# Kernel tuning notes

Measured on AMD Instinct MI355X. Metric: run time of the kernel, lower is better.

Reference implementation:

```python
import jax, jax.numpy as jnp
import numpy as np

COST_CLASS = 1.0
COST_MASK = 5.0
COST_DICE = 5.0


def _sample_points(masks, coords):
    """Bilinear grid_sample (align_corners=False, zero padding).

    masks:  [N, H, W] float
    coords: [P, 2] in [0, 1], (x, y) order as in torch grid_sample
    returns [N, P]
    """
    H, W = masks.shape[-2], masks.shape[-1]
    # torch: grid = 2*c - 1; pixel = ((grid+1)*size - 1)/2 = c*size - 0.5
    x = coords[:, 0] * W - 0.5
    y = coords[:, 1] * H - 0.5
    x0 = jnp.floor(x)
    y0 = jnp.floor(y)
    tx = (x - x0).astype(masks.dtype)
    ty = (y - y0).astype(masks.dtype)
    x0i = x0.astype(jnp.int32)
    y0i = y0.astype(jnp.int32)

    def gather(ix, iy):
        valid = ((ix >= 0) & (ix < W) & (iy >= 0) & (iy < H)).astype(masks.dtype)
        v = masks[:, jnp.clip(iy, 0, H - 1), jnp.clip(ix, 0, W - 1)]  # [N, P]
        return v * valid

    v00 = gather(x0i, y0i)
    v01 = gather(x0i + 1, y0i)
    v10 = gather(x0i, y0i + 1)
    v11 = gather(x0i + 1, y0i + 1)
    return (v00 * (1 - tx) * (1 - ty) + v01 * tx * (1 - ty)
            + v10 * (1 - tx) * ty + v11 * tx * ty)


def _cost_one(pred_mask, pred_logits, tgt_mask, labels, coords):
    # pred_mask [Q,H,W], pred_logits [Q,C], tgt_mask [T,H,W], labels [T], coords [P,2]
    probs = jax.nn.softmax(pred_logits, axis=-1)          # [Q, C]
    cost_class = -probs[:, labels]                        # [Q, T]

    pm = _sample_points(pred_mask, coords)                # [Q, P] logits
    tm = _sample_points(tgt_mask, coords)                 # [T, P] in [0,1]
    P = pm.shape[1]

    # pair-wise sigmoid BCE: BCE(x, 1) = softplus(-x), BCE(x, 0) = softplus(x)
    ce_pos = jax.nn.softplus(-pm) / P                     # [Q, P]
    ce_neg = jax.nn.softplus(pm) / P                      # [Q, P]
    cost_mask = ce_pos @ tm.T + ce_neg @ (1.0 - tm).T     # [Q, T]

    # pair-wise dice
    sig = jax.nn.sigmoid(pm)                              # [Q, P]
    numerator = 2.0 * (sig @ tm.T)                        # [Q, T]
    denominator = sig.sum(-1)[:, None] + tm.sum(-1)[None, :]
    cost_dice = 1.0 - (numerator + 1.0) / (denominator + 1.0)

    return COST_MASK * cost_mask + COST_CLASS * cost_class + COST_DICE * cost_dice


def setup_inputs() -> dict:
    key = jax.random.key(0)
    k1, k2, k3, k4, k5 = jax.random.split(key, 5)
    B, Q, C, T, H, W, P = 8, 150, 134, 32, 160, 160, 12544
    masks_queries_logits = jax.random.normal(k1, (B, Q, H, W), dtype=jnp.float32)
    class_queries_logits = jax.random.normal(k2, (B, Q, C), dtype=jnp.float32)
    # binary target masks
    mask_labels = (jax.random.uniform(k3, (B, T, H, W)) > 0.5).astype(jnp.float32)
    class_labels = jax.random.randint(k4, (B, T), 0, 133, dtype=jnp.int64)
    point_coords = jax.random.uniform(k5, (B, P, 2), dtype=jnp.float32)
    return {
        "masks_queries_logits": masks_queries_logits,
        "class_queries_logits": class_queries_logits,
        "mask_labels": mask_labels,
        "class_labels": class_labels,
        "point_coords": point_coords,
    }


def reference(masks_queries_logits, class_queries_logits, mask_labels, class_labels, point_coords):
    # Returns the per-sample cost matrices [B, Q, T] (the GPU-side work of the
    # matcher). The scipy Hungarian assignment on these matrices is CPU-bound
    # and intentionally excluded from the kernel baseline.
    cost = jax.vmap(_cost_one)(
        masks_queries_logits, class_queries_logits, mask_labels, class_labels, point_coords
    )
    return cost
```

## Files before the change

### kernel.cpp

```cpp
#include <hip/hip_runtime.h>
#include <hip/hip_bf16.h>
#include <hip/hip_fp16.h>
#include <math.h>

#define B_ 8
#define Q_ 150
#define QP_ 160
#define C_ 134
#define T_ 32
#define H_ 160
#define W_ 160
#define P_ 12544
#define HW_ (H_ * W_)
#define HW4_ (HW_ / 4)

#define SBLK 1024
#define SBATCH 3
#define STAIL 256
#define SEG_ 56
#define KSEG 224
#define KITER 7
#define DSTRIDE (2 * B_ * QP_ * T_)

typedef __attribute__((ext_vector_type(8))) short short8;
typedef __attribute__((ext_vector_type(4))) float floatx4;

struct Samp {
  int i00, i01, i10, i11;
  float w00, w01, w10, w11;
};

__device__ __forceinline__ Samp make_samp(float cx, float cy) {
  float x = cx * (float)W_ - 0.5f;
  float y = cy * (float)H_ - 0.5f;
  float x0f = floorf(x), y0f = floorf(y);
  float tx = x - x0f, ty = y - y0f;
  int x0 = (int)x0f, y0 = (int)y0f;
  int x1 = x0 + 1, y1 = y0 + 1;
  bool vx0 = (x0 >= 0) && (x0 < W_);
  bool vx1 = (x1 >= 0) && (x1 < W_);
  bool vy0 = (y0 >= 0) && (y0 < H_);
  bool vy1 = (y1 >= 0) && (y1 < H_);
  int cx0 = min(max(x0, 0), W_ - 1), cx1 = min(max(x1, 0), W_ - 1);
  int cy0 = min(max(y0, 0), H_ - 1), cy1 = min(max(y1, 0), H_ - 1);
  Samp s;
  s.i00 = cy0 * W_ + cx0;
  s.i01 = cy0 * W_ + cx1;
  s.i10 = cy1 * W_ + cx0;
  s.i11 = cy1 * W_ + cx1;
  float w00 = (1.f - tx) * (1.f - ty);
  float w01 = tx * (1.f - ty);
  float w10 = (1.f - tx) * ty;
  float w11 = tx * ty;
  s.w00 = (vx0 && vy0) ? w00 : 0.f;
  s.w01 = (vx1 && vy0) ? w01 : 0.f;
  s.w10 = (vx0 && vy1) ? w10 : 0.f;
  s.w11 = (vx1 && vy1) ? w11 : 0.f;
  return s;
}

__device__ __forceinline__ float waveSum(float v) {
#pragma unroll
  for (int m = 32; m >= 1; m >>= 1) v += __shfl_xor(v, m, 64);
  return v;
}
__device__ __forceinline__ float waveMax(float v) {
#pragma unroll
  for (int m = 32; m >= 1; m >>= 1) v = fmaxf(v, __shfl_xor(v, m, 64));
  return v;
}

__device__ __forceinline__ unsigned short f2bf(float x) {
  union { __hip_bfloat16 h; unsigned short u; } cv;
  cv.h = __float2bfloat16(x);
  return cv.u;
}
__device__ __forceinline__ float bf2f(unsigned short u) {
  return __uint_as_float(((unsigned int)u) << 16);
}
__device__ __forceinline__ float h2f(unsigned short u) {
  union { __half h; unsigned short u; } cv;
  cv.u = u;
  return __half2float(cv.h);
}
__device__ __forceinline__ unsigned short f2h(float x) {
  union { __half h; unsigned short u; } cv;
  cv.h = __float2half(x);
  return cv.u;
}

__launch_bounds__(256) __global__
void samp_kernel(const float* __restrict__ coords,
                 unsigned int* __restrict__ sIdx,
                 uint2* __restrict__ sW) {
  int i = blockIdx.x * 256 + threadIdx.x;
  float2 cc = ((const float2*)coords)[i];
  Samp s = make_samp(cc.x, cc.y);
  int dx = s.i01 - s.i00;
  int dy = (s.i10 != s.i00) ? 1 : 0;
  sIdx[i] = (unsigned)s.i00 | ((unsigned)dx << 15) | ((unsigned)dy << 16);
  uint2 w;
  w.x = (unsigned)f2h(s.w00) | ((unsigned)f2h(s.w01) << 16);
  w.y = (unsigned)f2h(s.w10) | ((unsigned)f2h(s.w11) << 16);
  sW[i] = w;
}

__device__ __forceinline__ float lds_sample(const unsigned short* img,
                                            unsigned iv, uint2 wv) {
  int i00 = iv & 0x7fff;
  int i01 = i00 + ((iv >> 15) & 1);
  int ir = (iv & 0x10000) ? W_ : 0;
  return h2f(wv.x & 0xffff) * bf2f(img[i00]) +
         h2f(wv.x >> 16) * bf2f(img[i01]) +
         h2f(wv.y & 0xffff) * bf2f(img[i00 + ir]) +
         h2f(wv.y >> 16) * bf2f(img[i01 + ir]);
}

__launch_bounds__(SBLK, 8) __global__
void sample_kernel(const float* __restrict__ masks_q,
                   const float* __restrict__ mask_labels,
                   const unsigned int* __restrict__ sIdx,
                   const uint2* __restrict__ sW,
                   unsigned short* __restrict__ pmh,
                   unsigned short* __restrict__ tmh,
                   float* __restrict__ S_sp, float* __restrict__ S_sig,
                   float* __restrict__ S_tm) {
  __shared__ unsigned short img[HW_];
  __shared__ float red[32];
  const int x = blockIdx.x;
  const int b = blockIdx.y;
  const int tid = threadIdx.x;
  const bool isPm = (x < Q_);

  const float* src = isPm ? (masks_q + ((size_t)b * Q_ + x) * HW_)
                          : (mask_labels + ((size_t)b * T_ + (x - Q_)) * HW_);
  const float4* s4 = (const float4*)src;
#pragma unroll
  for (int c = 0; c < 6; ++c) {
    int i = c * SBLK + tid;
    float4 v = s4[i];
    ushort4 u;
    u.x = f2bf(v.x); u.y = f2bf(v.y); u.z = f2bf(v.z); u.w = f2bf(v.w);
    *(ushort4*)&img[4 * i] = u;
  }
  if (tid < HW4_ - 6 * SBLK) {
    int i = 6 * SBLK + tid;
    float4 v = s4[i];
    ushort4 u;
    u.x = f2bf(v.x); u.y = f2bf(v.y); u.z = f2bf(v.z); u.w = f2bf(v.w);
    *(ushort4*)&img[4 * i] = u;
  }
  __syncthreads();

  const unsigned int* sIdxB = sIdx + (size_t)b * P_;
  const uint2* sWB = sW + (size_t)b * P_;

  if (isPm) {
    unsigned short* dst = pmh + ((size_t)b * QP_ + x) * P_;
    float ssp = 0.f, ssg = 0.f;
    for (int c = 0; c < SBATCH; ++c) {
      int p = c * (4 * SBLK) + tid;
      unsigned iv[4];
      uint2 wv[4];
      float v[4];
#pragma unroll
      for (int j = 0; j < 4; ++j) {
        iv[j] = sIdxB[p + j * SBLK];
        wv[j] = sWB[p + j * SBLK];
      }
#pragma unroll
      for (int j = 0; j < 4; ++j) v[j] = lds_sample(img, iv[j], wv[j]);
#pragma unroll
      for (int j = 0; j < 4; ++j) {
        float pm = v[j];
        float e = __expf(-fabsf(pm));
        float r = __builtin_amdgcn_rcpf(1.f + e);
        float sp = fmaxf(pm, 0.f) - __logf(r);
        float sg = (pm >= 0.f) ? r : e * r;
        ssp += sp;
        ssg += sg;
        dst[p + j * SBLK] = f2bf(pm);
      }
    }
    if (tid < STAIL) {
      int p = SBATCH * 4 * SBLK + tid;
      float pm = lds_sample(img, sIdxB[p], sWB[p]);
      float e = __expf(-fabsf(pm));
      float r = __builtin_amdgcn_rcpf(1.f + e);
      float sp = fmaxf(pm, 0.f) - __logf(r);
      float sg = (pm >= 0.f) ? r : e * r;
      ssp += sp;
      ssg += sg;
      dst[p] = f2bf(pm);
    }
    ssp = waveSum(ssp);
    ssg = waveSum(ssg);
    int w = tid >> 6;
    if ((tid & 63) == 0) {
      red[w] = ssp;
      red[16 + w] = ssg;
    }
    __syncthreads();
    if (tid == 0) {
      float a = 0.f, bb = 0.f;
#pragma unroll
      for (int i = 0; i < 16; ++i) { a += red[i]; bb += red[16 + i]; }
      S_sp[b * Q_ + x] = a;
      S_sig[b * Q_ + x] = bb;
    }
  } else {
    const int t = x - Q_;
    unsigned short* dst = tmh + ((size_t)b * T_ + t) * P_;
    float stm = 0.f;
    for (int c = 0; c < SBATCH; ++c) {
      int p = c * (4 * SBLK) + tid;
      unsigned iv[4];
      uint2 wv[4];
#pragma unroll
      for (int j = 0; j < 4; ++j) {
        iv[j] = sIdxB[p + j * SBLK];
        wv[j] = sWB[p + j * SBLK];
      }
#pragma unroll
      for (int j = 0; j < 4; ++j) {
        float v = lds_sample(img, iv[j], wv[j]);
        stm += v;
        dst[p + j * SBLK] = f2bf(v);
      }
    }
    if (tid < STAIL) {
      int p = SBATCH * 4 * SBLK + tid;
      float v = lds_sample(img, sIdxB[p], sWB[p]);
      stm += v;
      dst[p] = f2bf(v);
    }
    stm = waveSum(stm);
    int w = tid >> 6;
    if ((tid & 63) == 0) red[w] = stm;
    __syncthreads();
    if (tid == 0) {
      float a = 0.f;
#pragma unroll
      for (int i = 0; i < 16; ++i) a += red[i];
      S_tm[b * T_ + t] = a;
    }
  }
}

__device__ __forceinline__ short8 sig_frag(short8 a) {
  short8 out;
#pragma unroll
  for (int j = 0; j < 8; ++j) {
    float x = bf2f((unsigned short)a[j]);
    float e = __expf(-fabsf(x));
    float r = __builtin_amdgcn_rcpf(1.f + e);
    float sg = (x >= 0.f) ? r : e * r;
    out[j] = (short)f2bf(sg);
  }
  return out;
}

__launch_bounds__(320) __global__
void gemm_kernel(const unsigned short* __restrict__ pmh,
                 const unsigned short* __restrict__ tmh,
                 float* __restrict__ accP) {
  const int b = blockIdx.y;
  const int seg = blockIdx.x;
  const int w = threadIdx.x >> 6;
  const int l = threadIdx.x & 63;
  const int quad = l >> 4;
  const int mrow = l & 15;

  const unsigned short* pmb = pmh + ((size_t)b * QP_ + w * 32) * P_;
  const unsigned short* tmb = tmh + (size_t)b * T_ * P_;

  floatx4 aL[2][2];
  floatx4 aS[2][2];
#pragma unroll
  for (int i = 0; i < 2; ++i)
#pragma unroll
    for (int j = 0; j < 2; ++j) {
      aL[i][j] = (floatx4){0.f, 0.f, 0.f, 0.f};
      aS[i][j] = (floatx4){0.f, 0.f, 0.f, 0.f};
    }

  const int kbase = seg * KSEG;
#pragma unroll
  for (int ki = 0; ki < KITER; ++ki) {
    const int k0 = kbase + ki * 32 + quad * 8;
    short8 a0 = *(const short8*)(pmb + (size_t)(0 * 16 + mrow) * P_ + k0);
    short8 a1 = *(const short8*)(pmb + (size_t)(1 * 16 + mrow) * P_ + k0);
    short8 b0 = *(const short8*)(tmb + (size_t)(0 * 16 + mrow) * P_ + k0);
    short8 b1 = *(const short8*)(tmb + (size_t)(1 * 16 + mrow) * P_ + k0);
    short8 s0 = sig_frag(a0);
    short8 s1 = sig_frag(a1);
    aL[0][0] = __builtin_amdgcn_mfma_f32_16x16x32_bf16(a0, b0, aL[0][0], 0, 0, 0);
    aL[0][1] = __builtin_amdgcn_mfma_f32_16x16x32_bf16(a0, b1, aL[0][1], 0, 0, 0);
    aL[1][0] = __builtin_amdgcn_mfma_f32_16x16x32_bf16(a1, b0, aL[1][0], 0, 0, 0);
    aL[1][1] = __builtin_amdgcn_mfma_f32_16x16x32_bf16(a1, b1, aL[1][1], 0, 0, 0);
    aS[0][0] = __builtin_amdgcn_mfma_f32_16x16x32_bf16(s0, b0, aS[0][0], 0, 0, 0);
    aS[0][1] = __builtin_amdgcn_mfma_f32_16x16x32_bf16(s0, b1, aS[0][1], 0, 0, 0);
    aS[1][0] = __builtin_amdgcn_mfma_f32_16x16x32_bf16(s1, b0, aS[1][0], 0, 0, 0);
    aS[1][1] = __builtin_amdgcn_mfma_f32_16x16x32_bf16(s1, b1, aS[1][1], 0, 0, 0);
  }

  float* base = accP + (size_t)seg * DSTRIDE;
#pragma unroll
  for (int mtl = 0; mtl < 2; ++mtl)
#pragma unroll
    for (int nt = 0; nt < 2; ++nt)
#pragma unroll
      for (int r = 0; r < 4; ++r) {
        int q = w * 32 + mtl * 16 + quad * 4 + r;
        int t = nt * 16 + mrow;
        base[((size_t)(0 * B_ + b) * QP_ + q) * T_ + t] = aL[mtl][nt][r];
        base[((size_t)(1 * B_ + b) * QP_ + q) * T_ + t] = aS[mtl][nt][r];
      }
}

__launch_bounds__(256) __global__
void reduce_kernel(const float* __restrict__ accP, float* __restrict__ accD) {
  int i = blockIdx.x * 256 + threadIdx.x;
  float s = 0.f;
#pragma unroll
  for (int seg = 0; seg < SEG_; ++seg) s += accP[(size_t)seg * DSTRIDE + i];
  accD[i] = s;
}

__launch_bounds__(64) __global__
void final_kernel(const float* __restrict__ class_q,
                  const int* __restrict__ labels,
                  const float* __restrict__ accD,
                  const float* __restrict__ S_sp,
                  const float* __restrict__ S_sig,
                  const float* __restrict__ S_tm,
                  float* __restrict__ out) {
  const int bq = blockIdx.x;
  const int b = bq / Q_;
  const int q = bq % Q_;
  const int l = threadIdx.x;
  const float* cl = class_q + (size_t)bq * C_;

  float v = -INFINITY;
  for (int c = l; c < C_; c += 64) v = fmaxf(v, cl[c]);
  float m = waveMax(v);
  float e = 0.f;
  for (int c = l; c < C_; c += 64) e += __expf(cl[c] - m);
  float den = waveSum(e);

  if (l < T_) {
    int t = l;
    int lbl = labels[b * T_ + t];
    float prob = __expf(cl[lbl] - m) / den;
    float Dlin = accD[((size_t)(0 * B_ + b) * QP_ + q) * T_ + t];
    float Dsig = accD[((size_t)(1 * B_ + b) * QP_ + q) * T_ + t];
    float cmask = (S_sp[bq] - Dlin) * (1.f / (float)P_);
    float dice = 1.f - (2.f * Dsig + 1.f) / (S_sig[bq] + S_tm[b * T_ + t] + 1.f);
    out[(size_t)bq * T_ + t] = 5.f * cmask + 5.f * dice - prob;
  }
}

extern "C" void kernel_launch(void* const* d_in, const int* in_sizes, int n_in,
                              void* d_out, int out_size, void* d_ws,
                              size_t ws_size, hipStream_t stream) {
  const float* masks_q = (const float*)d_in[0];
  const float* class_q = (const float*)d_in[1];
  const float* mask_labels = (const float*)d_in[2];
  const int* class_labels = (const int*)d_in[3];
  const float* coords = (const float*)d_in[4];
  float* out = (float*)d_out;

  float* accD = (float*)d_ws;
  float* accP = accD + DSTRIDE;
  uint2* sW = (uint2*)(accP + (size_t)SEG_ * DSTRIDE);
  unsigned int* sIdx = (unsigned int*)(sW + (size_t)B_ * P_);
  float* S_sp = (float*)(sIdx + (size_t)B_ * P_);
  float* S_sig = S_sp + B_ * Q_;
  float* S_tm = S_sig + B_ * Q_;
  unsigned short* pmh = (unsigned short*)(S_tm + B_ * T_);
  unsigned short* tmh = pmh + (size_t)B_ * QP_ * P_;

  samp_kernel<<<(B_ * P_) / 256, 256, 0, stream>>>(coords, sIdx, sW);
  sample_kernel<<<dim3(Q_ + T_, B_), SBLK, 0, stream>>>(
      masks_q, mask_labels, sIdx, sW, pmh, tmh, S_sp, S_sig, S_tm);
  gemm_kernel<<<dim3(SEG_, B_), 320, 0, stream>>>(pmh, tmh, accP);
  reduce_kernel<<<DSTRIDE / 256, 256, 0, stream>>>(accP, accD);
  final_kernel<<<B_ * Q_, 64, 0, stream>>>(class_q, class_labels, accD, S_sp,
                                           S_sig, S_tm, out);
}
```

Baseline: 238.2 us.

## Store shifted bf16 image copy in LDS so bilinear taps need two 32-bit reads

The sample kernel now writes two bf16 copies of each mask into LDS, one shifted by a single element. Each horizontal pair of bilinear taps can then be fetched with one aligned 32-bit load, so a sample needs two LDS reads instead of four 16-bit reads. Sampling metadata is packed into a single uint4 holding a precomputed byte offset and the half-precision weights. The kernel also loads all 12 packed entries up front. The cost is double the LDS per block (about 100KB), which lowers occupancy (launch bound 8 down to 4), plus extra global reads while staging the image.

```diff
diff --git a/kernel.cpp b/kernel.cpp
--- a/kernel.cpp
+++ b/kernel.cpp
@@ -15,8 +15,9 @@
 #define HW4_ (HW_ / 4)
 
 #define SBLK 1024
-#define SBATCH 3
+#define NPT 12
 #define STAIL 256
+#define BOFS 51200
 #define SEG_ 56
 #define KSEG 224
 #define KITER 7
@@ -25,40 +26,6 @@
 typedef __attribute__((ext_vector_type(8))) short short8;
 typedef __attribute__((ext_vector_type(4))) float floatx4;
 
-struct Samp {
-  int i00, i01, i10, i11;
-  float w00, w01, w10, w11;
-};
-
-__device__ __forceinline__ Samp make_samp(float cx, float cy) {
-  float x = cx * (float)W_ - 0.5f;
-  float y = cy * (float)H_ - 0.5f;
-  float x0f = floorf(x), y0f = floorf(y);
-  float tx = x - x0f, ty = y - y0f;
-  int x0 = (int)x0f, y0 = (int)y0f;
-  int x1 = x0 + 1, y1 = y0 + 1;
-  bool vx0 = (x0 >= 0) && (x0 < W_);
-  bool vx1 = (x1 >= 0) && (x1 < W_);
-  bool vy0 = (y0 >= 0) && (y0 < H_);
-  bool vy1 = (y1 >= 0) && (y1 < H_);
-  int cx0 = min(max(x0, 0), W_ - 1), cx1 = min(max(x1, 0), W_ - 1);
-  int cy0 = min(max(y0, 0), H_ - 1), cy1 = min(max(y1, 0), H_ - 1);
-  Samp s;
-  s.i00 = cy0 * W_ + cx0;
-  s.i01 = cy0 * W_ + cx1;
-  s.i10 = cy1 * W_ + cx0;
-  s.i11 = cy1 * W_ + cx1;
-  float w00 = (1.f - tx) * (1.f - ty);
-  float w01 = tx * (1.f - ty);
-  float w10 = (1.f - tx) * ty;
-  float w11 = tx * ty;
-  s.w00 = (vx0 && vy0) ? w00 : 0.f;
-  s.w01 = (vx1 && vy0) ? w01 : 0.f;
-  s.w10 = (vx0 && vy1) ? w10 : 0.f;
-  s.w11 = (vx1 && vy1) ? w11 : 0.f;
-  return s;
-}
-
 __device__ __forceinline__ float waveSum(float v) {
 #pragma unroll
   for (int m = 32; m >= 1; m >>= 1) v += __shfl_xor(v, m, 64);
@@ -78,9 +45,9 @@
 __device__ __forceinline__ float bf2f(unsigned short u) {
   return __uint_as_float(((unsigned int)u) << 16);
 }
-__device__ __forceinline__ float h2f(unsigned short u) {
+__device__ __forceinline__ float h2f(unsigned u) {
   union { __half h; unsigned short u; } cv;
-  cv.u = u;
+  cv.u = (unsigned short)u;
   return __half2float(cv.h);
 }
 __device__ __forceinline__ unsigned short f2h(float x) {
@@ -91,41 +58,63 @@
 
 __launch_bounds__(256) __global__
 void samp_kernel(const float* __restrict__ coords,
-                 unsigned int* __restrict__ sIdx,
-                 uint2* __restrict__ sW) {
+                 uint4* __restrict__ sPack) {
   int i = blockIdx.x * 256 + threadIdx.x;
   float2 cc = ((const float2*)coords)[i];
-  Samp s = make_samp(cc.x, cc.y);
-  int dx = s.i01 - s.i00;
-  int dy = (s.i10 != s.i00) ? 1 : 0;
-  sIdx[i] = (unsigned)s.i00 | ((unsigned)dx << 15) | ((unsigned)dy << 16);
-  uint2 w;
-  w.x = (unsigned)f2h(s.w00) | ((unsigned)f2h(s.w01) << 16);
-  w.y = (unsigned)f2h(s.w10) | ((unsigned)f2h(s.w11) << 16);
-  sW[i] = w;
-}
-
-__device__ __forceinline__ float lds_sample(const unsigned short* img,
-                                            unsigned iv, uint2 wv) {
-  int i00 = iv & 0x7fff;
-  int i01 = i00 + ((iv >> 15) & 1);
-  int ir = (iv & 0x10000) ? W_ : 0;
-  return h2f(wv.x & 0xffff) * bf2f(img[i00]) +
-         h2f(wv.x >> 16) * bf2f(img[i01]) +
-         h2f(wv.y & 0xffff) * bf2f(img[i00 + ir]) +
-         h2f(wv.y >> 16) * bf2f(img[i01 + ir]);
-}
-
-__launch_bounds__(SBLK, 8) __global__
+  float x = cc.x * (float)W_ - 0.5f;
+  float y = cc.y * (float)H_ - 0.5f;
+  float x0f = floorf(x), y0f = floorf(y);
+  float tx = x - x0f, ty = y - y0f;
+  int x0 = (int)x0f, y0 = (int)y0f;
+
+  bool vx0 = (x0 >= 0) && (x0 < W_);
+  bool vx1 = (x0 + 1 >= 0) && (x0 + 1 < W_);
+  int bx; float wx0, wx1;
+  if (vx0) { bx = x0; wx0 = 1.f - tx; wx1 = vx1 ? tx : 0.f; }
+  else     { bx = min(max(x0 + 1, 0), W_ - 1); wx0 = vx1 ? tx : 0.f; wx1 = 0.f; }
+
+  bool vy0 = (y0 >= 0) && (y0 < H_);
+  bool vy1 = (y0 + 1 >= 0) && (y0 + 1 < H_);
+  int by, ir; float wy0, wy1;
+  if (vy0) {
+    by = y0; wy0 = 1.f - ty;
+    if (vy1) { wy1 = ty; ir = 1; } else { wy1 = 0.f; ir = 0; }
+  } else {
+    by = min(max(y0 + 1, 0), H_ - 1); wy0 = vy1 ? ty : 0.f; wy1 = 0.f; ir = 0;
+  }
+
+  int pi = by * W_ + bx;
+  unsigned off0 = (unsigned)((pi >> 1) * 4 + (pi & 1) * BOFS);
+  uint4 u;
+  u.x = off0 | (ir ? (320u << 17) : 0u);
+  u.y = (unsigned)f2h(wx0 * wy0) | ((unsigned)f2h(wx1 * wy0) << 16);
+  u.z = (unsigned)f2h(wx0 * wy1) | ((unsigned)f2h(wx1 * wy1) << 16);
+  u.w = 0u;
+  sPack[i] = u;
+}
+
+__device__ __forceinline__ float lds2(const unsigned short* img, uint4 pk) {
+  unsigned off0 = pk.x & 0x1ffffu;
+  unsigned off1 = off0 + (pk.x >> 17);
+  unsigned p0 = *(const unsigned*)((const char*)img + off0);
+  unsigned p1 = *(const unsigned*)((const char*)img + off1);
+  float v00 = __uint_as_float(p0 << 16);
+  float v01 = __uint_as_float(p0 & 0xffff0000u);
+  float v10 = __uint_as_float(p1 << 16);
+  float v11 = __uint_as_float(p1 & 0xffff0000u);
+  return h2f(pk.y & 0xffffu) * v00 + h2f(pk.y >> 16) * v01 +
+         h2f(pk.z & 0xffffu) * v10 + h2f(pk.z >> 16) * v11;
+}
+
+__launch_bounds__(SBLK, 4) __global__
 void sample_kernel(const float* __restrict__ masks_q,
                    const float* __restrict__ mask_labels,
-                   const unsigned int* __restrict__ sIdx,
-                   const uint2* __restrict__ sW,
+                   const uint4* __restrict__ sPack,
                    unsigned short* __restrict__ pmh,
                    unsigned short* __restrict__ tmh,
                    float* __restrict__ S_sp, float* __restrict__ S_sig,
                    float* __restrict__ S_tm) {
-  __shared__ unsigned short img[HW_];
+  __shared__ unsigned short img[2 * HW_];
   __shared__ float red[32];
   const int x = blockIdx.x;
   const int b = blockIdx.y;
@@ -139,57 +128,57 @@
   for (int c = 0; c < 6; ++c) {
     int i = c * SBLK + tid;
     float4 v = s4[i];
-    ushort4 u;
-    u.x = f2bf(v.x); u.y = f2bf(v.y); u.z = f2bf(v.z); u.w = f2bf(v.w);
-    *(ushort4*)&img[4 * i] = u;
+    float nxt = src[4 * i + 4];
+    ushort4 a;
+    a.x = f2bf(v.x); a.y = f2bf(v.y); a.z = f2bf(v.z); a.w = f2bf(v.w);
+    ushort4 bb;
+    bb.x = a.y; bb.y = a.z; bb.z = a.w; bb.w = f2bf(nxt);
+    *(ushort4*)&img[4 * i] = a;
+    *(ushort4*)&img[HW_ + 4 * i] = bb;
   }
   if (tid < HW4_ - 6 * SBLK) {
     int i = 6 * SBLK + tid;
     float4 v = s4[i];
-    ushort4 u;
-    u.x = f2bf(v.x); u.y = f2bf(v.y); u.z = f2bf(v.z); u.w = f2bf(v.w);
-    *(ushort4*)&img[4 * i] = u;
+    float nxt = (i < HW4_ - 1) ? src[4 * i + 4] : 0.f;
+    ushort4 a;
+    a.x = f2bf(v.x); a.y = f2bf(v.y); a.z = f2bf(v.z); a.w = f2bf(v.w);
+    ushort4 bb;
+    bb.x = a.y; bb.y = a.z; bb.z = a.w; bb.w = f2bf(nxt);
+    *(ushort4*)&img[4 * i] = a;
+    *(ushort4*)&img[HW_ + 4 * i] = bb;
   }
   __syncthreads();
 
-  const unsigned int* sIdxB = sIdx + (size_t)b * P_;
-  const uint2* sWB = sW + (size_t)b * P_;
+  const uint4* sp = sPack + (size_t)b * P_;
 
   if (isPm) {
     unsigned short* dst = pmh + ((size_t)b * QP_ + x) * P_;
     float ssp = 0.f, ssg = 0.f;
-    for (int c = 0; c < SBATCH; ++c) {
-      int p = c * (4 * SBLK) + tid;
-      unsigned iv[4];
-      uint2 wv[4];
-      float v[4];
-#pragma unroll
-      for (int j = 0; j < 4; ++j) {
-        iv[j] = sIdxB[p + j * SBLK];
-        wv[j] = sWB[p + j * SBLK];
-      }
-#pragma unroll
-      for (int j = 0; j < 4; ++j) v[j] = lds_sample(img, iv[j], wv[j]);
-#pragma unroll
-      for (int j = 0; j < 4; ++j) {
-        float pm = v[j];
-        float e = __expf(-fabsf(pm));
-        float r = __builtin_amdgcn_rcpf(1.f + e);
-        float sp = fmaxf(pm, 0.f) - __logf(r);
-        float sg = (pm >= 0.f) ? r : e * r;
-        ssp += sp;
-        ssg += sg;
-        dst[p + j * SBLK] = f2bf(pm);
-      }
-    }
-    if (tid < STAIL) {
-      int p = SBATCH * 4 * SBLK + tid;
-      float pm = lds_sample(img, sIdxB[p], sWB[p]);
+    uint4 pk[NPT];
+#pragma unroll
+    for (int j = 0; j < NPT; ++j) pk[j] = sp[j * SBLK + tid];
+    float v[NPT];
+#pragma unroll
+    for (int j = 0; j < NPT; ++j) v[j] = lds2(img, pk[j]);
+#pragma unroll
+    for (int j = 0; j < NPT; ++j) {
+      float pm = v[j];
       float e = __expf(-fabsf(pm));
       float r = __builtin_amdgcn_rcpf(1.f + e);
-      float sp = fmaxf(pm, 0.f) - __logf(r);
+      float sp_ = fmaxf(pm, 0.f) - __logf(r);
       float sg = (pm >= 0.f) ? r : e * r;
-      ssp += sp;
+      ssp += sp_;
+      ssg += sg;
+      dst[j * SBLK + tid] = f2bf(pm);
+    }
+    if (tid < STAIL) {
+      int p = NPT * SBLK + tid;
+      float pm = lds2(img, sp[p]);
+      float e = __expf(-fabsf(pm));
+      float r = __builtin_amdgcn_rcpf(1.f + e);
+      float sp_ = fmaxf(pm, 0.f) - __logf(r);
+      float sg = (pm >= 0.f) ? r : e * r;
+      ssp += sp_;
       ssg += sg;
       dst[p] = f2bf(pm);
     }
@@ -212,27 +201,22 @@
     const int t = x - Q_;
     unsigned short* dst = tmh + ((size_t)b * T_ + t) * P_;
     float stm = 0.f;
-    for (int c = 0; c < SBATCH; ++c) {
-      int p = c * (4 * SBLK) + tid;
-      unsigned iv[4];
-      uint2 wv[4];
-#pragma unroll
-      for (int j = 0; j < 4; ++j) {
-        iv[j] = sIdxB[p + j * SBLK];
-        wv[j] = sWB[p + j * SBLK];
-      }
-#pragma unroll
-      for (int j = 0; j < 4; ++j) {
-        float v = lds_sample(img, iv[j], wv[j]);
-        stm += v;
-        dst[p + j * SBLK] = f2bf(v);
-      }
+    uint4 pk[NPT];
+#pragma unroll
+    for (int j = 0; j < NPT; ++j) pk[j] = sp[j * SBLK + tid];
+    float v[NPT];
+#pragma unroll
+    for (int j = 0; j < NPT; ++j) v[j] = lds2(img, pk[j]);
+#pragma unroll
+    for (int j = 0; j < NPT; ++j) {
+      stm += v[j];
+      dst[j * SBLK + tid] = f2bf(v[j]);
     }
     if (tid < STAIL) {
-      int p = SBATCH * 4 * SBLK + tid;
-      float v = lds_sample(img, sIdxB[p], sWB[p]);
-      stm += v;
-      dst[p] = f2bf(v);
+      int p = NPT * SBLK + tid;
+      float vv = lds2(img, sp[p]);
+      stm += vv;
+      dst[p] = f2bf(vv);
     }
     stm = waveSum(stm);
     int w = tid >> 6;
@@ -372,17 +356,16 @@
 
   float* accD = (float*)d_ws;
   float* accP = accD + DSTRIDE;
-  uint2* sW = (uint2*)(accP + (size_t)SEG_ * DSTRIDE);
-  unsigned int* sIdx = (unsigned int*)(sW + (size_t)B_ * P_);
-  float* S_sp = (float*)(sIdx + (size_t)B_ * P_);
+  uint4* sPack = (uint4*)(accP + (size_t)SEG_ * DSTRIDE);
+  float* S_sp = (float*)(sPack + (size_t)B_ * P_);
   float* S_sig = S_sp + B_ * Q_;
   float* S_tm = S_sig + B_ * Q_;
   unsigned short* pmh = (unsigned short*)(S_tm + B_ * T_);
   unsigned short* tmh = pmh + (size_t)B_ * QP_ * P_;
 
-  samp_kernel<<<(B_ * P_) / 256, 256, 0, stream>>>(coords, sIdx, sW);
+  samp_kernel<<<(B_ * P_) / 256, 256, 0, stream>>>(coords, sPack);
   sample_kernel<<<dim3(Q_ + T_, B_), SBLK, 0, stream>>>(
-      masks_q, mask_labels, sIdx, sW, pmh, tmh, S_sp, S_sig, S_tm);
+      masks_q, mask_labels, sPack, pmh, tmh, S_sp, S_sig, S_tm);
   gemm_kernel<<<dim3(SEG_, B_), 320, 0, stream>>>(pmh, tmh, accP);
   reduce_kernel<<<DSTRIDE / 256, 256, 0, stream>>>(accP, accD);
   final_kernel<<<B_ * Q_, 64, 0, stream>>>(class_q, class_labels, accD, S_sp,
```

Measured after the change: 247.2 us. 3.8% more time.
